# Kernel tuning notes

Measured on AMD Instinct MI355X. Metric: run time of the kernel, lower is better.

The kernel has to match this reference:

```python
import jax, jax.numpy as jnp
import numpy as np

HID = 128
H = 96
W = 96
WS = 6      # window_size
SS = 3      # shift_size
LN_EPS = 1e-5


def _layer_norm(x, g, b):
    m = x.mean(-1, keepdims=True)
    v = ((x - m) ** 2).mean(-1, keepdims=True)
    return (x - m) / jnp.sqrt(v + LN_EPS) * g + b


def _block(x, Wm, bm, g, bg):
    # Linear -> LayerNorm -> GELU (dropout is identity at inference)
    return jax.nn.gelu(_layer_norm(x @ Wm + bm, g, bg), approximate=False)


def _window_context(grid, Wt, bt, gt, bgt):
    # grid: [B, H, W, D]. Window partition + mean over the ws*ws tokens is
    # equivalent to a mean over each (ws, ws) tile; broadcasting back is a repeat.
    B, Hh, Ww, D = grid.shape
    nh, nw = Hh // WS, Ww // WS
    win_mean = grid.reshape(B, nh, WS, nw, WS, D).mean(axis=(2, 4))  # [B, nh, nw, D]
    tok = _block(win_mean, Wt, bt, gt, bgt)                          # token_proj
    return jnp.repeat(jnp.repeat(tok, WS, axis=1), WS, axis=2)       # [B, H, W, D]


def setup_inputs() -> dict:
    key = jax.random.key(0)
    ks = jax.random.split(key, 8)
    B = 32
    s = 1.0 / np.sqrt(HID)
    inp = {
        "h_pixel": jax.random.normal(ks[0], (B, H * W, HID), dtype=jnp.float32),
        "node_mask": jnp.ones((B, H * W), dtype=jnp.float32),
        # token_proj: Linear(D,D) + LayerNorm(D)
        "Wt": jax.random.normal(ks[1], (HID, HID), dtype=jnp.float32) * s,
        "bt": jnp.zeros((HID,), jnp.float32),
        "gt": jnp.ones((HID,), jnp.float32),
        "bgt": jnp.zeros((HID,), jnp.float32),
        # fuse: Linear(D,D) + LayerNorm(D)  (regular_shifted_sum -> fuse_in = D)
        "Wf": jax.random.normal(ks[2], (HID, HID), dtype=jnp.float32) * s,
        "bf": jnp.zeros((HID,), jnp.float32),
        "gf": jnp.ones((HID,), jnp.float32),
        "bgf": jnp.zeros((HID,), jnp.float32),
        # out_proj: Linear(D,D) + LayerNorm(D)
        "Wo": jax.random.normal(ks[3], (HID, HID), dtype=jnp.float32) * s,
        "bo": jnp.zeros((HID,), jnp.float32),
        "go": jnp.ones((HID,), jnp.float32),
        "bgo": jnp.zeros((HID,), jnp.float32),
    }
    return inp


def reference(h_pixel, node_mask, Wt, bt, gt, bgt, Wf, bf, gf, bgf, Wo, bo, go, bgo):
    B, N, D = h_pixel.shape
    grid = h_pixel.reshape(B, H, W, D)
    reg = _window_context(grid, Wt, bt, gt, bgt)
    shifted = jnp.roll(grid, (-SS, -SS), axis=(1, 2))
    sh = _window_context(shifted, Wt, bt, gt, bgt)
    sh = jnp.roll(sh, (SS, SS), axis=(1, 2))
    ctx = _block(reg + sh, Wf, bf, gf, bgf)     # fuse
    out = _block(ctx, Wo, bo, go, bgo)          # out_proj
    out = out.reshape(B, N, D) * node_mask[..., None]
    return out
```

## Files before the change

### kernel.cpp

```cpp
#include <hip/hip_runtime.h>
#include <hip/hip_bf16.h>


#define DEVFN static __device__ __forceinline__

typedef __attribute__((ext_vector_type(8))) short bf16x8;
typedef __attribute__((ext_vector_type(16))) float f32x16;

DEVFN float gelu_fast(float x) {
  const float u = 1.5957691216057308f * (x + 0.044715f * x * x * x);
  return x / (1.0f + __expf(-u));
}

DEVFN unsigned short f2bf(float f) {
  unsigned int u = __float_as_uint(f);
  u = (u + 0x7FFFu + ((u >> 16) & 1u)) >> 16;
  return (unsigned short)u;
}

DEVFN float bf2f(unsigned short u) {
  return __uint_as_float((unsigned int)u << 16);
}

DEVFN void add4(float4& a, const float4 v) {
  a.x += v.x; a.y += v.y; a.z += v.z; a.w += v.w;
}
DEVFN void fma4(float4& a, const float4 v, float m) {
  a.x = fmaf(v.x, m, a.x); a.y = fmaf(v.y, m, a.y);
  a.z = fmaf(v.z, m, a.z); a.w = fmaf(v.w, m, a.w);
}

__global__ __launch_bounds__(512) void k_tile3(const float* __restrict__ h,
                                               unsigned short* __restrict__ S3) {
  const int b  = blockIdx.x >> 5;
  const int ry = blockIdx.x & 31;
  const int w    = threadIdx.x >> 6;
  const int lane = threadIdx.x & 63;
  const int half = lane >> 5;
  const int ch4  = (lane & 31) << 2;
  const float mlo = half ? 0.f : 1.f;
  const float mhi = 1.f - mlo;

  float4 acc[4];
  #pragma unroll
  for (int t = 0; t < 4; ++t) acc[t] = make_float4(0.f, 0.f, 0.f, 0.f);

  #pragma unroll
  for (int yy = 0; yy < 3; ++yy) {
    const float* rp =
        h + ((size_t)(b * 9216 + (3 * ry + yy) * 96 + 12 * w + half) * 128 + ch4);
    #pragma unroll
    for (int j = 0; j < 6; ++j) {
      const float4 v = *reinterpret_cast<const float4*>(rp + j * 256);
      if (j == 0)      add4(acc[0], v);
      else if (j == 2) add4(acc[1], v);
      else if (j == 3) add4(acc[2], v);
      else if (j == 5) add4(acc[3], v);
      else if (j == 1) { fma4(acc[0], v, mlo); fma4(acc[1], v, mhi); }
      else             { fma4(acc[2], v, mlo); fma4(acc[3], v, mhi); }
    }
  }

  #pragma unroll
  for (int t = 0; t < 4; ++t) {
    float4 s = acc[t];
    s.x += __shfl_xor(s.x, 32, 64);
    s.y += __shfl_xor(s.y, 32, 64);
    s.z += __shfl_xor(s.z, 32, 64);
    s.w += __shfl_xor(s.w, 32, 64);
    if (half == 0) {
      short4 pk;
      pk.x = (short)f2bf(s.x); pk.y = (short)f2bf(s.y);
      pk.z = (short)f2bf(s.z); pk.w = (short)f2bf(s.w);
      *reinterpret_cast<short4*>(
          &S3[((size_t)(b * 32 + ry) * 32 + 4 * w + t) * 128 + ch4]) = pk;
    }
  }
}

DEVFN void stage_w_bf(unsigned short* __restrict__ wl,
                      const float* __restrict__ W, int tid) {
  #pragma unroll
  for (int p = 0; p < 4; ++p) {
    const int i = tid + p * 512;
    const int kp = i >> 5;
    const int n4 = (i & 31) * 4;
    const float4 r0 = *reinterpret_cast<const float4*>(W + (size_t)(2 * kp) * 128 + n4);
    const float4 r1 = *reinterpret_cast<const float4*>(W + (size_t)(2 * kp + 1) * 128 + n4);
    const float a0[4] = {r0.x, r0.y, r0.z, r0.w};
    const float a1[4] = {r1.x, r1.y, r1.z, r1.w};
    #pragma unroll
    for (int j = 0; j < 4; ++j) {
      const unsigned int pk =
          (unsigned int)f2bf(a0[j]) | ((unsigned int)f2bf(a1[j]) << 16);
      *reinterpret_cast<unsigned int*>(&wl[(n4 + j) * 136 + 2 * kp]) = pk;
    }
  }
}

DEVFN f32x16 mfma_tile(const unsigned short* __restrict__ xrow,
                       const unsigned short* __restrict__ wrow) {
  f32x16 acc;
  #pragma unroll
  for (int r = 0; r < 16; ++r) acc[r] = 0.f;
  #pragma unroll
  for (int kk = 0; kk < 8; ++kk) {
    const bf16x8 a = *reinterpret_cast<const bf16x8*>(xrow + kk * 16);
    const bf16x8 bb = *reinterpret_cast<const bf16x8*>(wrow + kk * 16);
    acc = __builtin_amdgcn_mfma_f32_32x32x16_bf16(a, bb, acc, 0, 0, 0);
  }
  return acc;
}

DEVFN void write_raw(float* __restrict__ raw, const f32x16 acc,
                     int tg, int cg, int lane) {
  const int n  = cg * 32 + (lane & 31);
  const int mb = tg * 32 + 4 * (lane >> 5);
  #pragma unroll
  for (int r = 0; r < 16; ++r) {
    const int mm = mb + (r & 3) + 8 * (r >> 2);
    raw[mm * 132 + n] = acc[r];
  }
}

__global__ __launch_bounds__(512) void k_tok(const unsigned short* __restrict__ S3,
    const float* __restrict__ Wt, const float* __restrict__ bt,
    const float* __restrict__ gt, const float* __restrict__ bgt,
    float* __restrict__ tok) {
  __shared__ __align__(16) unsigned short xs_bf[64 * 136];
  __shared__ __align__(16) unsigned short wl[128 * 136];
  float* raw = reinterpret_cast<float*>(wl);

  const int tid = threadIdx.x;
  const int t0 = blockIdx.x * 64;
  const int s  = t0 >> 13;
  const int b  = (t0 >> 8) & 31;
  const int wyx = t0 & 255;

  const unsigned short* Sb = S3 + (size_t)b * 131072;
  #pragma unroll
  for (int p = 0; p < 2; ++p) {
    const int i = tid + p * 512;
    const int tt = i >> 4, c8 = (i & 15) * 8;
    const int idx = wyx + tt;
    const int wy = idx >> 4, wx = idx & 15;
    int ry0, ry1, c0, c1;
    if (s == 0) { ry0 = 2 * wy;     ry1 = 2 * wy + 1;        c0 = 2 * wx;     c1 = 2 * wx + 1; }
    else        { ry0 = 2 * wy + 1; ry1 = (2 * wy + 2) & 31; c0 = 2 * wx + 1; c1 = (2 * wx + 2) & 31; }
    const bf16x8 v00 = *reinterpret_cast<const bf16x8*>(Sb + ((size_t)(ry0 * 32 + c0) * 128 + c8));
    const bf16x8 v01 = *reinterpret_cast<const bf16x8*>(Sb + ((size_t)(ry0 * 32 + c1) * 128 + c8));
    const bf16x8 v10 = *reinterpret_cast<const bf16x8*>(Sb + ((size_t)(ry1 * 32 + c0) * 128 + c8));
    const bf16x8 v11 = *reinterpret_cast<const bf16x8*>(Sb + ((size_t)(ry1 * 32 + c1) * 128 + c8));
    bf16x8 pk;
    #pragma unroll
    for (int j = 0; j < 8; ++j) {
      const float sum = bf2f((unsigned short)v00[j]) + bf2f((unsigned short)v01[j]) +
                        bf2f((unsigned short)v10[j]) + bf2f((unsigned short)v11[j]);
      pk[j] = (short)f2bf(sum * (1.f / 36.f));
    }
    *reinterpret_cast<bf16x8*>(&xs_bf[tt * 136 + c8]) = pk;
  }
  stage_w_bf(wl, Wt, tid);
  __syncthreads();

  const int lane = tid & 63;
  const int w = tid >> 6;
  const int tg = w >> 2, cg = w & 3;
  const unsigned short* xrow = &xs_bf[(tg * 32 + (lane & 31)) * 136 + 8 * (lane >> 5)];
  const unsigned short* wrow = &wl[(cg * 32 + (lane & 31)) * 136 + 8 * (lane >> 5)];

  const f32x16 acc = mfma_tile(xrow, wrow);
  __syncthreads();
  write_raw(raw, acc, tg, cg, lane);
  __syncthreads();

  {
    const int tt = tid >> 3, cb = tid & 7;
    float v[16];
    float s2 = 0.f, q = 0.f;
    #pragma unroll
    for (int i = 0; i < 4; ++i) {
      const int col = 4 * cb + 32 * i;
      const float4 rv = *reinterpret_cast<const float4*>(&raw[tt * 132 + col]);
      const float4 bv = *reinterpret_cast<const float4*>(bt + col);
      v[4 * i + 0] = rv.x + bv.x; v[4 * i + 1] = rv.y + bv.y;
      v[4 * i + 2] = rv.z + bv.z; v[4 * i + 3] = rv.w + bv.w;
    }
    #pragma unroll
    for (int e = 0; e < 16; ++e) { s2 += v[e]; q += v[e] * v[e]; }
    s2 += __shfl_xor(s2, 1, 8); q += __shfl_xor(q, 1, 8);
    s2 += __shfl_xor(s2, 2, 8); q += __shfl_xor(q, 2, 8);
    s2 += __shfl_xor(s2, 4, 8); q += __shfl_xor(q, 4, 8);
    const float mean = s2 * (1.f / 128.f);
    const float var  = q * (1.f / 128.f) - mean * mean;
    const float inv  = rsqrtf(var + 1e-5f);
    #pragma unroll
    for (int i = 0; i < 4; ++i) {
      const int col = 4 * cb + 32 * i;
      const float4 gv = *reinterpret_cast<const float4*>(gt + col);
      const float4 ev = *reinterpret_cast<const float4*>(bgt + col);
      float4 ov;
      ov.x = gelu_fast((v[4 * i + 0] - mean) * inv * gv.x + ev.x);
      ov.y = gelu_fast((v[4 * i + 1] - mean) * inv * gv.y + ev.y);
      ov.z = gelu_fast((v[4 * i + 2] - mean) * inv * gv.z + ev.z);
      ov.w = gelu_fast((v[4 * i + 3] - mean) * inv * gv.w + ev.w);
      *reinterpret_cast<float4*>(tok + (size_t)(t0 + tt) * 128 + col) = ov;
    }
  }
}

__global__ __launch_bounds__(512) void k_fuse_out(const float* __restrict__ tok,
    const float* __restrict__ Wf, const float* __restrict__ bfv,
    const float* __restrict__ gf, const float* __restrict__ bgf,
    const float* __restrict__ Wo, const float* __restrict__ bo,
    const float* __restrict__ go, const float* __restrict__ bgo,
    const float* __restrict__ mask, float* __restrict__ out) {
  __shared__ __align__(16) unsigned short xs_bf[64 * 136];
  __shared__ __align__(16) unsigned short wl[128 * 136];
  float* raw = reinterpret_cast<float*>(wl);

  const int tid = threadIdx.x;
  const int b = blockIdx.x >> 4;
  const int m = blockIdx.x & 15;
  const int lane = tid & 63;
  const int w = tid >> 6;
  const int tg = w >> 2, cg = w & 3;

  const float* tokR = tok + (size_t)b * 32768 + (size_t)m * 2048;
  const float* tokS = tok + 1048576 + (size_t)b * 32768;

  #pragma unroll
  for (int p = 0; p < 2; ++p) {
    const int i = tid + p * 512;
    const int t = i >> 4, c8 = (i & 15) * 8;
    const int gx = t & 31, gy = 2 * m + (t >> 5);
    const int wx  = gx >> 1;
    const int wxs = ((gx + 31) & 31) >> 1;
    const int wys = ((gy + 31) & 31) >> 1;
    const float* pr = tokR + (size_t)wx * 128 + c8;
    const float* ps = tokS + (size_t)(wys * 16 + wxs) * 128 + c8;
    bf16x8 pk;
    #pragma unroll
    for (int j = 0; j < 8; ++j)
      pk[j] = (short)f2bf(pr[j] + ps[j]);
    *reinterpret_cast<bf16x8*>(&xs_bf[t * 136 + c8]) = pk;
  }
  stage_w_bf(wl, Wf, tid);
  __syncthreads();

  const unsigned short* xrow = &xs_bf[(tg * 32 + (lane & 31)) * 136 + 8 * (lane >> 5)];
  const unsigned short* wrow = &wl[(cg * 32 + (lane & 31)) * 136 + 8 * (lane >> 5)];

  const f32x16 acc1 = mfma_tile(xrow, wrow);
  __syncthreads();
  write_raw(raw, acc1, tg, cg, lane);
  __syncthreads();

  {
    const int tt = tid >> 3, cb = tid & 7;
    float v[16];
    float s = 0.f, q = 0.f;
    #pragma unroll
    for (int i = 0; i < 4; ++i) {
      const int col = 4 * cb + 32 * i;
      const float4 rv = *reinterpret_cast<const float4*>(&raw[tt * 132 + col]);
      const float4 bv = *reinterpret_cast<const float4*>(bfv + col);
      v[4 * i + 0] = rv.x + bv.x; v[4 * i + 1] = rv.y + bv.y;
      v[4 * i + 2] = rv.z + bv.z; v[4 * i + 3] = rv.w + bv.w;
    }
    #pragma unroll
    for (int e = 0; e < 16; ++e) { s += v[e]; q += v[e] * v[e]; }
    s += __shfl_xor(s, 1, 8); q += __shfl_xor(q, 1, 8);
    s += __shfl_xor(s, 2, 8); q += __shfl_xor(q, 2, 8);
    s += __shfl_xor(s, 4, 8); q += __shfl_xor(q, 4, 8);
    const float mean = s * (1.f / 128.f);
    const float var  = q * (1.f / 128.f) - mean * mean;
    const float inv  = rsqrtf(var + 1e-5f);
    #pragma unroll
    for (int i = 0; i < 4; ++i) {
      const int col = 4 * cb + 32 * i;
      const float4 gv = *reinterpret_cast<const float4*>(gf + col);
      const float4 ev = *reinterpret_cast<const float4*>(bgf + col);
      short4 pk;
      pk.x = (short)f2bf(gelu_fast((v[4 * i + 0] - mean) * inv * gv.x + ev.x));
      pk.y = (short)f2bf(gelu_fast((v[4 * i + 1] - mean) * inv * gv.y + ev.y));
      pk.z = (short)f2bf(gelu_fast((v[4 * i + 2] - mean) * inv * gv.z + ev.z));
      pk.w = (short)f2bf(gelu_fast((v[4 * i + 3] - mean) * inv * gv.w + ev.w));
      *reinterpret_cast<short4*>(&xs_bf[tt * 136 + col]) = pk;
    }
  }
  __syncthreads();
  stage_w_bf(wl, Wo, tid);
  __syncthreads();

  const f32x16 acc2 = mfma_tile(xrow, wrow);
  __syncthreads();
  write_raw(raw, acc2, tg, cg, lane);
  __syncthreads();

  {
    const int tt = tid >> 3, cb = tid & 7;
    float v[16];
    float s = 0.f, q = 0.f;
    #pragma unroll
    for (int i = 0; i < 4; ++i) {
      const int col = 4 * cb + 32 * i;
      const float4 rv = *reinterpret_cast<const float4*>(&raw[tt * 132 + col]);
      const float4 bv = *reinterpret_cast<const float4*>(bo + col);
      v[4 * i + 0] = rv.x + bv.x; v[4 * i + 1] = rv.y + bv.y;
      v[4 * i + 2] = rv.z + bv.z; v[4 * i + 3] = rv.w + bv.w;
    }
    #pragma unroll
    for (int e = 0; e < 16; ++e) { s += v[e]; q += v[e] * v[e]; }
    s += __shfl_xor(s, 1, 8); q += __shfl_xor(q, 1, 8);
    s += __shfl_xor(s, 2, 8); q += __shfl_xor(q, 2, 8);
    s += __shfl_xor(s, 4, 8); q += __shfl_xor(q, 4, 8);
    const float mean = s * (1.f / 128.f);
    const float var  = q * (1.f / 128.f) - mean * mean;
    const float inv  = rsqrtf(var + 1e-5f);
    #pragma unroll
    for (int i = 0; i < 4; ++i) {
      const int col = 4 * cb + 32 * i;
      const float4 gv = *reinterpret_cast<const float4*>(go + col);
      const float4 ev = *reinterpret_cast<const float4*>(bgo + col);
      v[4 * i + 0] = gelu_fast((v[4 * i + 0] - mean) * inv * gv.x + ev.x);
      v[4 * i + 1] = gelu_fast((v[4 * i + 1] - mean) * inv * gv.y + ev.y);
      v[4 * i + 2] = gelu_fast((v[4 * i + 2] - mean) * inv * gv.z + ev.z);
      v[4 * i + 3] = gelu_fast((v[4 * i + 3] - mean) * inv * gv.w + ev.w);
    }
    const int gx = tt & 31, gy = 2 * m + (tt >> 5);
    #pragma unroll
    for (int py = 0; py < 3; ++py) {
      const int y = 3 * gy + py;
      #pragma unroll
      for (int px = 0; px < 3; ++px) {
        const int x = 3 * gx + px;
        const size_t pix = (size_t)b * 9216 + (size_t)y * 96 + x;
        const float mv = mask[pix];
        #pragma unroll
        for (int i = 0; i < 4; ++i) {
          const int col = 4 * cb + 32 * i;
          *reinterpret_cast<float4*>(out + pix * 128 + col) =
              make_float4(v[4 * i + 0] * mv, v[4 * i + 1] * mv,
                          v[4 * i + 2] * mv, v[4 * i + 3] * mv);
        }
      }
    }
  }
}

extern "C" void kernel_launch(void* const* d_in, const int* in_sizes, int n_in,
                              void* d_out, int out_size, void* d_ws, size_t ws_size,
                              hipStream_t stream) {
  (void)in_sizes; (void)n_in; (void)out_size; (void)ws_size;
  const float* h    = (const float*)d_in[0];
  const float* mask = (const float*)d_in[1];
  const float* Wt   = (const float*)d_in[2];
  const float* bt   = (const float*)d_in[3];
  const float* gt   = (const float*)d_in[4];
  const float* bgt  = (const float*)d_in[5];
  const float* Wf   = (const float*)d_in[6];
  const float* bfv  = (const float*)d_in[7];
  const float* gf   = (const float*)d_in[8];
  const float* bgf  = (const float*)d_in[9];
  const float* Wo   = (const float*)d_in[10];
  const float* bo   = (const float*)d_in[11];
  const float* go   = (const float*)d_in[12];
  const float* bgo  = (const float*)d_in[13];

  unsigned short* S3 = (unsigned short*)d_ws;
  float* tok = (float*)((char*)d_ws + (size_t)8 * 1024 * 1024);
  float* out = (float*)d_out;

  hipLaunchKernelGGL(k_tile3, dim3(1024), dim3(512), 0, stream, h, S3);
  hipLaunchKernelGGL(k_tok, dim3(256), dim3(512), 0, stream,
                     S3, Wt, bt, gt, bgt, tok);
  hipLaunchKernelGGL(k_fuse_out, dim3(512), dim3(512), 0, stream,
                     tok, Wf, bfv, gf, bgf, Wo, bo, go, bgo, mask, out);
}
```

Measured before the change: 88.16 us.

## Store token intermediate in bf16, use hardware bf16 pack and nontemporal stores

Replaces the software round-to-nearest bf16 conversion with the v_cvt_pk_bf16_f32 instruction, which packs two floats per op. Changes the token buffer between k_tok and k_fuse_out from fp32 to bf16, halving that intermediate traffic. Adds nontemporal stores for the S3, token and final output writes so they bypass cache retention. Risks slight precision change from rounding tok to bf16 before the add, and possible NaN/rounding semantic differences of the hardware convert.

```diff
diff --git a/kernel.cpp b/kernel.cpp
--- a/kernel.cpp
+++ b/kernel.cpp
@@ -6,16 +6,18 @@
 
 typedef __attribute__((ext_vector_type(8))) short bf16x8;
 typedef __attribute__((ext_vector_type(16))) float f32x16;
+typedef __attribute__((ext_vector_type(2))) unsigned int uintx2;
+typedef __attribute__((ext_vector_type(4))) float floatx4;
 
 DEVFN float gelu_fast(float x) {
   const float u = 1.5957691216057308f * (x + 0.044715f * x * x * x);
   return x / (1.0f + __expf(-u));
 }
 
-DEVFN unsigned short f2bf(float f) {
-  unsigned int u = __float_as_uint(f);
-  u = (u + 0x7FFFu + ((u >> 16) & 1u)) >> 16;
-  return (unsigned short)u;
+DEVFN unsigned int cvt_pk_bf16(float lo, float hi) {
+  unsigned int r;
+  asm("v_cvt_pk_bf16_f32 %0, %1, %2" : "=v"(r) : "v"(lo), "v"(hi));
+  return r;
 }
 
 DEVFN float bf2f(unsigned short u) {
@@ -69,11 +71,11 @@
     s.z += __shfl_xor(s.z, 32, 64);
     s.w += __shfl_xor(s.w, 32, 64);
     if (half == 0) {
-      short4 pk;
-      pk.x = (short)f2bf(s.x); pk.y = (short)f2bf(s.y);
-      pk.z = (short)f2bf(s.z); pk.w = (short)f2bf(s.w);
-      *reinterpret_cast<short4*>(
-          &S3[((size_t)(b * 32 + ry) * 32 + 4 * w + t) * 128 + ch4]) = pk;
+      uintx2 pk;
+      pk.x = cvt_pk_bf16(s.x, s.y);
+      pk.y = cvt_pk_bf16(s.z, s.w);
+      __builtin_nontemporal_store(pk, reinterpret_cast<uintx2*>(
+          &S3[((size_t)(b * 32 + ry) * 32 + 4 * w + t) * 128 + ch4]));
     }
   }
 }
@@ -91,9 +93,8 @@
     const float a1[4] = {r1.x, r1.y, r1.z, r1.w};
     #pragma unroll
     for (int j = 0; j < 4; ++j) {
-      const unsigned int pk =
-          (unsigned int)f2bf(a0[j]) | ((unsigned int)f2bf(a1[j]) << 16);
-      *reinterpret_cast<unsigned int*>(&wl[(n4 + j) * 136 + 2 * kp]) = pk;
+      *reinterpret_cast<unsigned int*>(&wl[(n4 + j) * 136 + 2 * kp]) =
+          cvt_pk_bf16(a0[j], a1[j]);
     }
   }
 }
@@ -126,7 +127,7 @@
 __global__ __launch_bounds__(512) void k_tok(const unsigned short* __restrict__ S3,
     const float* __restrict__ Wt, const float* __restrict__ bt,
     const float* __restrict__ gt, const float* __restrict__ bgt,
-    float* __restrict__ tok) {
+    unsigned short* __restrict__ tok) {
   __shared__ __align__(16) unsigned short xs_bf[64 * 136];
   __shared__ __align__(16) unsigned short wl[128 * 136];
   float* raw = reinterpret_cast<float*>(wl);
@@ -151,14 +152,16 @@
     const bf16x8 v01 = *reinterpret_cast<const bf16x8*>(Sb + ((size_t)(ry0 * 32 + c1) * 128 + c8));
     const bf16x8 v10 = *reinterpret_cast<const bf16x8*>(Sb + ((size_t)(ry1 * 32 + c0) * 128 + c8));
     const bf16x8 v11 = *reinterpret_cast<const bf16x8*>(Sb + ((size_t)(ry1 * 32 + c1) * 128 + c8));
-    bf16x8 pk;
+    float sv[8];
     #pragma unroll
     for (int j = 0; j < 8; ++j) {
-      const float sum = bf2f((unsigned short)v00[j]) + bf2f((unsigned short)v01[j]) +
-                        bf2f((unsigned short)v10[j]) + bf2f((unsigned short)v11[j]);
-      pk[j] = (short)f2bf(sum * (1.f / 36.f));
-    }
-    *reinterpret_cast<bf16x8*>(&xs_bf[tt * 136 + c8]) = pk;
+      sv[j] = (bf2f((unsigned short)v00[j]) + bf2f((unsigned short)v01[j]) +
+               bf2f((unsigned short)v10[j]) + bf2f((unsigned short)v11[j])) * (1.f / 36.f);
+    }
+    unsigned int* dst = reinterpret_cast<unsigned int*>(&xs_bf[tt * 136 + c8]);
+    #pragma unroll
+    for (int j = 0; j < 4; ++j)
+      dst[j] = cvt_pk_bf16(sv[2 * j], sv[2 * j + 1]);
   }
   stage_w_bf(wl, Wt, tid);
   __syncthreads();
@@ -199,17 +202,20 @@
       const int col = 4 * cb + 32 * i;
       const float4 gv = *reinterpret_cast<const float4*>(gt + col);
       const float4 ev = *reinterpret_cast<const float4*>(bgt + col);
-      float4 ov;
-      ov.x = gelu_fast((v[4 * i + 0] - mean) * inv * gv.x + ev.x);
-      ov.y = gelu_fast((v[4 * i + 1] - mean) * inv * gv.y + ev.y);
-      ov.z = gelu_fast((v[4 * i + 2] - mean) * inv * gv.z + ev.z);
-      ov.w = gelu_fast((v[4 * i + 3] - mean) * inv * gv.w + ev.w);
-      *reinterpret_cast<float4*>(tok + (size_t)(t0 + tt) * 128 + col) = ov;
-    }
-  }
-}
-
-__global__ __launch_bounds__(512) void k_fuse_out(const float* __restrict__ tok,
+      const float o0 = gelu_fast((v[4 * i + 0] - mean) * inv * gv.x + ev.x);
+      const float o1 = gelu_fast((v[4 * i + 1] - mean) * inv * gv.y + ev.y);
+      const float o2 = gelu_fast((v[4 * i + 2] - mean) * inv * gv.z + ev.z);
+      const float o3 = gelu_fast((v[4 * i + 3] - mean) * inv * gv.w + ev.w);
+      uintx2 pk;
+      pk.x = cvt_pk_bf16(o0, o1);
+      pk.y = cvt_pk_bf16(o2, o3);
+      __builtin_nontemporal_store(pk, reinterpret_cast<uintx2*>(
+          tok + (size_t)(t0 + tt) * 128 + col));
+    }
+  }
+}
+
+__global__ __launch_bounds__(512) void k_fuse_out(const unsigned short* __restrict__ tok,
     const float* __restrict__ Wf, const float* __restrict__ bfv,
     const float* __restrict__ gf, const float* __restrict__ bgf,
     const float* __restrict__ Wo, const float* __restrict__ bo,
@@ -226,8 +232,8 @@
   const int w = tid >> 6;
   const int tg = w >> 2, cg = w & 3;
 
-  const float* tokR = tok + (size_t)b * 32768 + (size_t)m * 2048;
-  const float* tokS = tok + 1048576 + (size_t)b * 32768;
+  const unsigned short* tokR = tok + (size_t)b * 32768 + (size_t)m * 2048;
+  const unsigned short* tokS = tok + 1048576 + (size_t)b * 32768;
 
   #pragma unroll
   for (int p = 0; p < 2; ++p) {
@@ -237,13 +243,16 @@
     const int wx  = gx >> 1;
     const int wxs = ((gx + 31) & 31) >> 1;
     const int wys = ((gy + 31) & 31) >> 1;
-    const float* pr = tokR + (size_t)wx * 128 + c8;
-    const float* ps = tokS + (size_t)(wys * 16 + wxs) * 128 + c8;
-    bf16x8 pk;
+    const bf16x8 pr = *reinterpret_cast<const bf16x8*>(tokR + (size_t)wx * 128 + c8);
+    const bf16x8 ps = *reinterpret_cast<const bf16x8*>(tokS + (size_t)(wys * 16 + wxs) * 128 + c8);
+    float sv[8];
     #pragma unroll
     for (int j = 0; j < 8; ++j)
-      pk[j] = (short)f2bf(pr[j] + ps[j]);
-    *reinterpret_cast<bf16x8*>(&xs_bf[t * 136 + c8]) = pk;
+      sv[j] = bf2f((unsigned short)pr[j]) + bf2f((unsigned short)ps[j]);
+    unsigned int* dst = reinterpret_cast<unsigned int*>(&xs_bf[t * 136 + c8]);
+    #pragma unroll
+    for (int j = 0; j < 4; ++j)
+      dst[j] = cvt_pk_bf16(sv[2 * j], sv[2 * j + 1]);
   }
   stage_w_bf(wl, Wf, tid);
   __syncthreads();
@@ -281,12 +290,14 @@
       const int col = 4 * cb + 32 * i;
       const float4 gv = *reinterpret_cast<const float4*>(gf + col);
       const float4 ev = *reinterpret_cast<const float4*>(bgf + col);
-      short4 pk;
-      pk.x = (short)f2bf(gelu_fast((v[4 * i + 0] - mean) * inv * gv.x + ev.x));
-      pk.y = (short)f2bf(gelu_fast((v[4 * i + 1] - mean) * inv * gv.y + ev.y));
-      pk.z = (short)f2bf(gelu_fast((v[4 * i + 2] - mean) * inv * gv.z + ev.z));
-      pk.w = (short)f2bf(gelu_fast((v[4 * i + 3] - mean) * inv * gv.w + ev.w));
-      *reinterpret_cast<short4*>(&xs_bf[tt * 136 + col]) = pk;
+      const float o0 = gelu_fast((v[4 * i + 0] - mean) * inv * gv.x + ev.x);
+      const float o1 = gelu_fast((v[4 * i + 1] - mean) * inv * gv.y + ev.y);
+      const float o2 = gelu_fast((v[4 * i + 2] - mean) * inv * gv.z + ev.z);
+      const float o3 = gelu_fast((v[4 * i + 3] - mean) * inv * gv.w + ev.w);
+      uintx2 pk;
+      pk.x = cvt_pk_bf16(o0, o1);
+      pk.y = cvt_pk_bf16(o2, o3);
+      *reinterpret_cast<uintx2*>(&xs_bf[tt * 136 + col]) = pk;
     }
   }
   __syncthreads();
@@ -340,9 +351,11 @@
         #pragma unroll
         for (int i = 0; i < 4; ++i) {
           const int col = 4 * cb + 32 * i;
-          *reinterpret_cast<float4*>(out + pix * 128 + col) =
-              make_float4(v[4 * i + 0] * mv, v[4 * i + 1] * mv,
-                          v[4 * i + 2] * mv, v[4 * i + 3] * mv);
+          floatx4 ov;
+          ov.x = v[4 * i + 0] * mv; ov.y = v[4 * i + 1] * mv;
+          ov.z = v[4 * i + 2] * mv; ov.w = v[4 * i + 3] * mv;
+          __builtin_nontemporal_store(ov,
+              reinterpret_cast<floatx4*>(out + pix * 128 + col));
         }
       }
     }
@@ -368,8 +381,8 @@
   const float* go   = (const float*)d_in[12];
   const float* bgo  = (const float*)d_in[13];
 
-  unsigned short* S3 = (unsigned short*)d_ws;
-  float* tok = (float*)((char*)d_ws + (size_t)8 * 1024 * 1024);
+  unsigned short* S3  = (unsigned short*)d_ws;
+  unsigned short* tok = (unsigned short*)((char*)d_ws + (size_t)8 * 1024 * 1024);
   float* out = (float*)d_out;
 
   hipLaunchKernelGGL(k_tile3, dim3(1024), dim3(512), 0, stream, h, S3);
```

After: 76.35 us. 13.4% less time.
